# Kernel optimization log

Measured on AMD Instinct MI355X. Metric: run time of the kernel, lower is better.

## Reference

```python
import jax, jax.numpy as jnp
import numpy as np

J, P, L, C = 24, 8, 128, 8
N = 65536


def grid_sample(image, grid):
    # Bilinear grid_sample, align_corners=True, border-clamped indices
    # image: (B, C, H, W), grid: (B, Hg, Wg, 2) with (x=width, y=height) in [-1, 1]
    B, Cc, H, W = image.shape
    Hg, Wg = grid.shape[1], grid.shape[2]
    ix = (grid[..., 0] + 1.0) * 0.5 * (W - 1)
    iy = (grid[..., 1] + 1.0) * 0.5 * (H - 1)
    ix0 = jnp.floor(ix)
    iy0 = jnp.floor(iy)
    ix1 = ix0 + 1.0
    iy1 = iy0 + 1.0
    w_nw = (ix1 - ix) * (iy1 - iy)
    w_ne = (ix - ix0) * (iy1 - iy)
    w_sw = (ix1 - ix) * (iy - iy0)
    w_se = (ix - ix0) * (iy - iy0)
    ix0c = jnp.clip(ix0, 0, W - 1).astype(jnp.int32)
    ix1c = jnp.clip(ix1, 0, W - 1).astype(jnp.int32)
    iy0c = jnp.clip(iy0, 0, H - 1).astype(jnp.int32)
    iy1c = jnp.clip(iy1, 0, H - 1).astype(jnp.int32)
    img = image.reshape(B, Cc, H * W)

    def gather(iyc, ixc):
        idx = (iyc * W + ixc).reshape(B, 1, Hg * Wg)
        return jnp.take_along_axis(img, idx, axis=2)  # (B, Cc, Hg*Wg)

    out = (gather(iy0c, ix0c) * w_nw.reshape(B, 1, -1)
           + gather(iy0c, ix1c) * w_ne.reshape(B, 1, -1)
           + gather(iy1c, ix0c) * w_sw.reshape(B, 1, -1)
           + gather(iy1c, ix1c) * w_se.reshape(B, 1, -1))
    return out.reshape(B, Cc, Hg, Wg)


def sample(feat_lines, grid, pid):
    # feat_lines: (J, P, Lh, Lw, C); grid: (1, N, 1, 2)
    Jn, Pn, Lh, Lw, Cn = feat_lines.shape
    B, Np = grid.shape[:2]
    lines = jnp.transpose(feat_lines[:, pid], (0, 3, 1, 2)).reshape(1, Jn * Cn, Lh, Lw)
    feat = grid_sample(lines, grid)  # (1, J*C, N, 1)
    # raw reshape, replicating torch .view(B, N, J, C) on contiguous (1, J*C, N, 1)
    return feat.reshape(B, Np, Jn, Cn)


def setup_inputs():
    key = jax.random.key(0)
    ks = jax.random.split(key, 5)
    s = 0.01
    return {
        "feat_lines_x": jax.random.uniform(ks[0], (J, P, L, L, C), jnp.float32, -s, s),
        "feat_lines_y": jax.random.uniform(ks[1], (J, P, L, L, C), jnp.float32, -s, s),
        "feat_lines_z": jax.random.uniform(ks[2], (J, P, L, L, C), jnp.float32, -s, s),
        "query_points": jax.random.uniform(ks[3], (N, 3), jnp.float32),
        "scale": jnp.ones((3,), jnp.float32),
        "skinning_weight": jax.random.uniform(ks[4], (N, J), jnp.float32),
        "id": 3,
    }


def reference(feat_lines_x, feat_lines_y, feat_lines_z, query_points, scale, skinning_weight, id):
    qp = query_points - jnp.mean(query_points, axis=0)[None, :]  # (N, 3)
    x = qp[:, 0] / (scale[0] / 2)
    y = qp[:, 1] / (scale[1] / 2)
    z = qp[:, 2] / (scale[2] / 2)
    yx = jnp.stack((y, x), axis=1)[None, :, None, :]  # (1, N, 1, 2)
    xz = jnp.stack((x, z), axis=1)[None, :, None, :]
    zy = jnp.stack((z, y), axis=1)[None, :, None, :]
    feat_x = sample(feat_lines_x, yx, id)
    feat_y = sample(feat_lines_y, zy, id)
    feat_z = sample(feat_lines_z, xz, id)
    feat = jnp.concatenate([feat_x, feat_y, feat_z], axis=3)  # (1, N, J, 3C)
    return jnp.einsum('bnjc,nj->bnc', feat, skinning_weight)  # (1, N, 3C)
```

## Files before the change

### kernel.cpp

```cpp
#include <hip/hip_runtime.h>

constexpr int NPQ = 65536;
constexpr int JJ = 24, CC = 8, PP = 8, LL = 128;
constexpr int OUTC = 24;
constexpr int TOTAL = NPQ * OUTC;
constexpr int NCHP = 192;
constexpr size_t QPL = 8192;
constexpr size_t Q_ELEMS = (size_t)576 * QPL;

typedef _Float16 h2 __attribute__((ext_vector_type(2)));

constexpr float QSCALE = 12750.0f;
constexpr float QBIASF = 128.0f;
constexpr float INVQ = 1.0f / 12750.0f;

__global__ __launch_bounds__(256) void k_prep_all(
    const float* __restrict__ fx_, const float* __restrict__ fy_,
    const float* __restrict__ fz_, const int* __restrict__ idp,
    const float* __restrict__ qp, const float* __restrict__ sw,
    unsigned short* __restrict__ Q16, unsigned short* __restrict__ swh,
    float* __restrict__ partial) {
    int bid = blockIdx.x;
    int t = threadIdx.x;
    if (bid < 2304) {
        int g = bid >> 5;
        int rg = bid & 31;
        int p = g / 24, jimg = g - p * 24;
        const float* feat = (p == 0) ? fx_ : (p == 1) ? fy_ : fz_;
        int pid = *idp;
        int ly = t >> 6, k = t & 63;
        int y = rg * 4 + ly;
        int x2 = k * 2;
        const float* src = feat + (((size_t)jimg * PP + (size_t)pid) * 16384 +
                                   (size_t)(y * 128 + x2)) * 8;
        float4 a0 = *(const float4*)src;
        float4 a1 = *(const float4*)(src + 4);
        float4 b0 = *(const float4*)(src + 8);
        float4 b1 = *(const float4*)(src + 12);
        float av[8] = {a0.x, a0.y, a0.z, a0.w, a1.x, a1.y, a1.z, a1.w};
        float bv[8] = {b0.x, b0.y, b0.z, b0.w, b1.x, b1.y, b1.z, b1.w};
#pragma unroll
        for (int c = 0; c < 8; ++c) {
            unsigned qa = (unsigned)fmaf(av[c], QSCALE, QBIASF);
            unsigned qb = (unsigned)fmaf(bv[c], QSCALE, QBIASF);
            Q16[((size_t)(g * 8 + c) << 13) + (size_t)(y * 64 + k)] =
                (unsigned short)(qa | (qb << 8));
        }
    } else if (bid < 2560) {
        __shared__ float s[3][256];
        int n = (bid - 2304) * 256 + t;
        s[0][t] = qp[n * 3 + 0];
        s[1][t] = qp[n * 3 + 1];
        s[2][t] = qp[n * 3 + 2];
        __syncthreads();
        for (int off = 128; off > 0; off >>= 1) {
            if (t < off) {
                s[0][t] += s[0][t + off];
                s[1][t] += s[1][t + off];
                s[2][t] += s[2][t + off];
            }
            __syncthreads();
        }
        if (t == 0) {
            partial[(bid - 2304) * 4 + 0] = s[0][0];
            partial[(bid - 2304) * 4 + 1] = s[1][0];
            partial[(bid - 2304) * 4 + 2] = s[2][0];
        }
    } else {
        int n = (bid - 2560) * 256 + t;
        const float* s = sw + (size_t)n * 24;
        float4 v0 = *(const float4*)(s);
        float4 v1 = *(const float4*)(s + 4);
        float4 v2 = *(const float4*)(s + 8);
        float4 v3 = *(const float4*)(s + 12);
        float4 v4 = *(const float4*)(s + 16);
        float4 v5 = *(const float4*)(s + 20);
        float vv[24] = {v0.x, v0.y, v0.z, v0.w, v1.x, v1.y, v1.z, v1.w,
                        v2.x, v2.y, v2.z, v2.w, v3.x, v3.y, v3.z, v3.w,
                        v4.x, v4.y, v4.z, v4.w, v5.x, v5.y, v5.z, v5.w};
        unsigned u[12];
#pragma unroll
        for (int q = 0; q < 12; ++q) {
            h2 w;
            w[0] = (_Float16)vv[q * 2];
            w[1] = (_Float16)vv[q * 2 + 1];
            u[q] = __builtin_bit_cast(unsigned, w);
        }
        uint4* dst = (uint4*)(swh + (size_t)n * 24);
        dst[0] = make_uint4(u[0], u[1], u[2], u[3]);
        dst[1] = make_uint4(u[4], u[5], u[6], u[7]);
        dst[2] = make_uint4(u[8], u[9], u[10], u[11]);
    }
}

__global__ __launch_bounds__(256) void k_coord(
    const float* __restrict__ qp, const float* __restrict__ scale,
    const float* __restrict__ partial, unsigned int* __restrict__ co,
    float* __restrict__ out) {
    __shared__ float s[3][256];
    __shared__ float smean[3];
    int t = threadIdx.x;
    s[0][t] = partial[t * 4 + 0];
    s[1][t] = partial[t * 4 + 1];
    s[2][t] = partial[t * 4 + 2];
    __syncthreads();
    for (int off = 128; off > 0; off >>= 1) {
        if (t < off) {
            s[0][t] += s[0][t + off];
            s[1][t] += s[1][t + off];
            s[2][t] += s[2][t + off];
        }
        __syncthreads();
    }
    if (t < 3) smean[t] = s[t][0] * (1.0f / 65536.0f);
    __syncthreads();

    int gt = blockIdx.x * 256 + t;
    if (gt < 3 * 191 * 8) {
        int c = gt & 7;
        int rest = gt >> 3;
        int jcb = rest % 191;
        int p = rest / 191;
        if (((jcb + 1) % 3) != 0) {
            int np = ((jcb + 1) << 16) / 192;
            out[(size_t)np * 24 + p * 8 + c] = 0.0f;
        }
    }

    int n = blockIdx.x * 256 + t;
    float qv[3] = {qp[n * 3 + 0], qp[n * 3 + 1], qp[n * 3 + 2]};
#pragma unroll
    for (int p = 0; p < 3; ++p) {
        int wc = (p + 1) - ((p + 1) >= 3 ? 3 : 0);
        int hc = p;
        float gw = (qv[wc] - smean[wc]) * (2.0f / scale[wc]);
        float gh = (qv[hc] - smean[hc]) * (2.0f / scale[hc]);
        float ixf = (gw + 1.0f) * 63.5f;
        float iyf = (gh + 1.0f) * 63.5f;
        float fx0 = floorf(ixf), fy0 = floorf(iyf);
        float fx = ixf - fx0, fy = iyf - fy0;
        int x0i = (int)fx0, y0i = (int)fy0;
        int xr, yr;
        float fxc, fyc;
        if (x0i < 0)        { xr = 0;   fxc = 0.0f; }
        else if (x0i > 126) { xr = 126; fxc = 1.0f; }
        else                { xr = x0i; fxc = fx;   }
        if (y0i < 0)        { yr = 0;   fyc = 0.0f; }
        else if (y0i > 126) { yr = 126; fyc = 1.0f; }
        else                { yr = y0i; fyc = fy;   }
        unsigned fxq = (unsigned)__float2int_rn(fxc * 511.0f);
        unsigned fyq = (unsigned)__float2int_rn(fyc * 511.0f);
        co[((size_t)p << 16) + (size_t)n] =
            (unsigned)(yr * 128 + xr) | (fxq << 14) | (fyq << 23);
    }
}

__device__ __forceinline__ float sample1(const unsigned int* sp, unsigned d) {
    unsigned w = sp[d & 16383u];
    float fx = (float)((d >> 14) & 511u) * (1.0f / 511.0f);
    float fy = (float)(d >> 23) * (1.0f / 511.0f);
    float v00 = (float)(w & 255u);
    float v01 = (float)((w >> 8) & 255u);
    float v10 = (float)((w >> 16) & 255u);
    float v11 = (float)(w >> 24);
    float r0 = fmaf(fy, v10 - v00, v00);
    float r1 = fmaf(fy, v11 - v01, v01);
    return fmaf(fx, r1 - r0, r0);
}

__device__ __forceinline__ void up2(float* d, unsigned u) {
    h2 v = __builtin_bit_cast(h2, u);
    d[0] = (float)v[0];
    d[1] = (float)v[1];
}

__global__ __launch_bounds__(512, 4) void k_fused(
    const unsigned short* __restrict__ Q16, const unsigned int* __restrict__ co,
    const unsigned short* __restrict__ swh, float* __restrict__ out) {
    int b = blockIdx.x;
    int Lid = (b & 7) * 144 + (b >> 3);
    int half = Lid & 1;
    int jcp = Lid >> 1;
    int p = jcp / NCHP;
    int jc = jcp - p * NCHP;

    __shared__ unsigned int splane[16384];
    {
        const unsigned int* src32 =
            (const unsigned int*)(Q16 + ((size_t)jcp << 13));
        int tid = threadIdx.x;
#pragma unroll
        for (int it = 0; it < 8; ++it) {
            int i = it * 512 + tid;
            int y = i >> 5;
            int m = i & 31;
            int ip1 = (m < 31) ? i + 1 : i;
            int ro = (y < 127) ? 32 : 0;
            unsigned c0 = src32[i];
            unsigned c1 = src32[ip1];
            unsigned n0 = src32[i + ro];
            unsigned n1 = src32[ip1 + ro];
            unsigned w0 = __builtin_amdgcn_perm(n0, c0, 0x05040100u);
            unsigned w1 = __builtin_amdgcn_perm(n0, c0, 0x06050201u);
            unsigned w2 = __builtin_amdgcn_perm(n0, c0, 0x07060302u);
            unsigned selA = (m < 31) ? 0x00000403u : 0x00000303u;
            unsigned t0 = __builtin_amdgcn_perm(c1, c0, selA);
            unsigned t1 = __builtin_amdgcn_perm(n1, n0, selA);
            unsigned w3 = __builtin_amdgcn_perm(t1, t0, 0x05040100u);
            ((uint4*)splane)[i] = make_uint4(w0, w1, w2, w3);
        }
    }
    __syncthreads();
    const unsigned int* sp = splane;

    int i0 = jc << 16;
    int r  = (jc % 3) * 64;
    int r1 = ((jc + 1) % 3) * 64;
    int npF_lo = (i0 + 191) / 192;
    int npF_hi = ((jc + 1) << 16) / 192;
    int cnt = npF_hi - npF_lo;
    int mid = npF_lo + (cnt >> 1);
    int loR = half ? mid : npF_lo;
    int hiR = half ? npF_hi : mid;
    bool hasPre  = (half == 0) && (r != 0);
    bool hasPost = (half == 1) && (r1 != 0);

    int nFull = (hiR - loR) * 8;
    int nTot = nFull + (hasPre ? 8 : 0) + (hasPost ? 8 : 0);
    const unsigned int* cop = co + ((size_t)p << 16);

    for (int k = threadIdx.x; k < nTot; k += 512) {
        if (k < nFull) {
            int np = loR + (k >> 3);
            int c = k & 7;
            const unsigned int* cb = cop + (np * 192 + c - i0);
            const uint4* sw4 = (const uint4*)(swh + (size_t)np * 24);
            uint4 wA = sw4[0], wB = sw4[1], wC = sw4[2];
            float swreg[24];
            up2(swreg + 0,  wA.x); up2(swreg + 2,  wA.y);
            up2(swreg + 4,  wA.z); up2(swreg + 6,  wA.w);
            up2(swreg + 8,  wB.x); up2(swreg + 10, wB.y);
            up2(swreg + 12, wB.z); up2(swreg + 14, wB.w);
            up2(swreg + 16, wC.x); up2(swreg + 18, wC.y);
            up2(swreg + 20, wC.z); up2(swreg + 22, wC.w);
            float sumw = 0.0f;
#pragma unroll
            for (int j = 0; j < 24; ++j) sumw += swreg[j];
            float acc = 0.0f;
#pragma unroll
            for (int j = 0; j < 24; ++j) {
                unsigned d = cb[j * 8];
                acc = fmaf(swreg[j], sample1(sp, d), acc);
            }
            out[(size_t)np * 24 + p * 8 + c] = fmaf(acc, INVQ, -sumw * 0.01f);
        } else {
            bool isPre = hasPre && (k < nFull + 8);
            int c = (k - nFull) & 7;
            int np = isPre ? (i0 / 192) : npF_hi;
            int jlo = isPre ? (r >> 3) : 0;
            int jhi = isPre ? 24 : (r1 >> 3);
            int n0 = np * 192 + c - i0;
            float acc = 0.0f, sumw = 0.0f;
            for (int j = jlo; j < jhi; ++j) {
                unsigned d = cop[n0 + j * 8];
                float wj =
                    (float)__builtin_bit_cast(_Float16, swh[(size_t)np * 24 + j]);
                sumw += wj;
                acc = fmaf(wj, sample1(sp, d), acc);
            }
            atomicAdd(&out[(size_t)np * 24 + p * 8 + c],
                      fmaf(acc, INVQ, -sumw * 0.01f));
        }
    }
}

__global__ __launch_bounds__(256) void k_partial(const float* __restrict__ qp,
                                                 float* __restrict__ partial) {
    __shared__ float s[3][256];
    int t = threadIdx.x;
    int n = blockIdx.x * 256 + t;
    s[0][t] = qp[n * 3 + 0];
    s[1][t] = qp[n * 3 + 1];
    s[2][t] = qp[n * 3 + 2];
    __syncthreads();
    for (int off = 128; off > 0; off >>= 1) {
        if (t < off) {
            s[0][t] += s[0][t + off];
            s[1][t] += s[1][t + off];
            s[2][t] += s[2][t + off];
        }
        __syncthreads();
    }
    if (t == 0) {
        partial[blockIdx.x * 4 + 0] = s[0][0];
        partial[blockIdx.x * 4 + 1] = s[1][0];
        partial[blockIdx.x * 4 + 2] = s[2][0];
    }
}

__global__ __launch_bounds__(256) void k_finalm(const float* __restrict__ partial,
                                                float* __restrict__ mean) {
    __shared__ float s[3][256];
    int t = threadIdx.x;
    s[0][t] = partial[t * 4 + 0];
    s[1][t] = partial[t * 4 + 1];
    s[2][t] = partial[t * 4 + 2];
    __syncthreads();
    for (int off = 128; off > 0; off >>= 1) {
        if (t < off) {
            s[0][t] += s[0][t + off];
            s[1][t] += s[1][t + off];
            s[2][t] += s[2][t + off];
        }
        __syncthreads();
    }
    if (t < 3) mean[t] = s[t][0] * (1.0f / 65536.0f);
}

__global__ __launch_bounds__(256) void k_main(
    const float* __restrict__ featx, const float* __restrict__ featy,
    const float* __restrict__ featz, const float* __restrict__ qp,
    const float* __restrict__ scale, const float* __restrict__ sw,
    const int* __restrict__ idp, const float* __restrict__ mean,
    float* __restrict__ out) {
    int t = blockIdx.x * 256 + threadIdx.x;
    if (t >= TOTAL) return;
    int np = t / OUTC;
    int cp = t - np * OUTC;
    int p  = cp >> 3;
    int c  = cp & 7;
    const float* feat = (p == 0) ? featx : (p == 1) ? featy : featz;
    int pid = *idp;
    int wc = (p + 1) - ((p + 1) >= 3 ? 3 : 0);
    int hc = p;
    float mw = mean[wc], mh = mean[hc];
    float invw = 2.0f / scale[wc];
    float invh = 2.0f / scale[hc];
    const float* featpid = feat + (size_t)pid * (LL * LL * CC);
    int ibase = np * 192 + c;
    float acc = 0.0f;
#pragma unroll 4
    for (int j = 0; j < JJ; ++j) {
        int i  = ibase + j * 8;
        int jc = i >> 16;
        int n  = i & 65535;
        int jimg = jc >> 3;
        int cimg = jc & 7;
        const float* img = featpid + (size_t)jimg * (PP * LL * LL * CC) + cimg;
        float gw = (qp[n * 3 + wc] - mw) * invw;
        float gh = (qp[n * 3 + hc] - mh) * invh;
        float ixf = (gw + 1.0f) * 63.5f;
        float iyf = (gh + 1.0f) * 63.5f;
        float ix0 = floorf(ixf), iy0 = floorf(iyf);
        float fx = ixf - ix0, fy = iyf - iy0;
        int x0i = (int)ix0, y0i = (int)iy0;
        int x0 = min(127, max(0, x0i));
        int x1 = min(127, max(0, x0i + 1));
        int y0 = min(127, max(0, y0i));
        int y1 = min(127, max(0, y0i + 1));
        int r0 = y0 * (LL * CC);
        int r1 = y1 * (LL * CC);
        float v00 = img[r0 + x0 * CC];
        float v01 = img[r0 + x1 * CC];
        float v10 = img[r1 + x0 * CC];
        float v11 = img[r1 + x1 * CC];
        float omfx = 1.0f - fx, omfy = 1.0f - fy;
        float S = omfx * omfy * v00 + fx * omfy * v01 +
                  omfx * fy * v10 + fx * fy * v11;
        acc += sw[np * JJ + j] * S;
    }
    out[t] = acc;
}

extern "C" void kernel_launch(void* const* d_in, const int* in_sizes, int n_in,
                              void* d_out, int out_size, void* d_ws, size_t ws_size,
                              hipStream_t stream) {
    const float* featx = (const float*)d_in[0];
    const float* featy = (const float*)d_in[1];
    const float* featz = (const float*)d_in[2];
    const float* qp    = (const float*)d_in[3];
    const float* scale = (const float*)d_in[4];
    const float* sw    = (const float*)d_in[5];
    const int*   idp   = (const int*)d_in[6];
    float* out = (float*)d_out;

    size_t off_Q = 0;
    size_t off_co = off_Q + Q_ELEMS * 2;
    size_t off_sw = off_co + (size_t)3 * 65536 * 4;
    size_t off_partial = off_sw + (size_t)65536 * 24 * 2;
    size_t off_mean = off_partial + 4096;
    size_t needed = off_mean + 16;

    if (ws_size >= needed) {
        char* wsb = (char*)d_ws;
        unsigned short* Q16 = (unsigned short*)(wsb + off_Q);
        unsigned int* co    = (unsigned int*)(wsb + off_co);
        unsigned short* swh = (unsigned short*)(wsb + off_sw);
        float* partial      = (float*)(wsb + off_partial);

        k_prep_all<<<2816, 256, 0, stream>>>(featx, featy, featz, idp, qp, sw,
                                             Q16, swh, partial);
        k_coord<<<256, 256, 0, stream>>>(qp, scale, partial, co, out);
        k_fused<<<1152, 512, 0, stream>>>(Q16, co, swh, out);
    } else {
        float* ws = (float*)d_ws;
        float* mean    = ws;
        float* partial = ws + 4;
        k_partial<<<256, 256, 0, stream>>>(qp, partial);
        k_finalm<<<1, 256, 0, stream>>>(partial, mean);
        k_main<<<(TOTAL + 255) / 256, 256, 0, stream>>>(
            featx, featy, featz, qp, scale, sw, idp, mean, out);
    }
}
```

Baseline: 52.28 us.

## Shrink shared plane to 16-bit horizontal pairs and use one block per plane

```diff
diff --git a/kernel.cpp b/kernel.cpp
--- a/kernel.cpp
+++ b/kernel.cpp
@@ -155,14 +155,16 @@
     }
 }
 
-__device__ __forceinline__ float sample1(const unsigned int* sp, unsigned d) {
-    unsigned w = sp[d & 16383u];
+__device__ __forceinline__ float sample1(const unsigned short* sq, unsigned d) {
+    unsigned widx = d & 16383u;
+    unsigned w0 = sq[widx];
+    unsigned w1 = sq[widx + 128];
     float fx = (float)((d >> 14) & 511u) * (1.0f / 511.0f);
     float fy = (float)(d >> 23) * (1.0f / 511.0f);
-    float v00 = (float)(w & 255u);
-    float v01 = (float)((w >> 8) & 255u);
-    float v10 = (float)((w >> 16) & 255u);
-    float v11 = (float)(w >> 24);
+    float v00 = (float)(w0 & 255u);
+    float v01 = (float)(w0 >> 8);
+    float v10 = (float)(w1 & 255u);
+    float v11 = (float)(w1 >> 8);
     float r0 = fmaf(fy, v10 - v00, v00);
     float r1 = fmaf(fy, v11 - v01, v01);
     return fmaf(fx, r1 - r0, r0);
@@ -174,64 +176,46 @@
     d[1] = (float)v[1];
 }
 
-__global__ __launch_bounds__(512, 4) void k_fused(
+__global__ __launch_bounds__(256, 3) void k_fused(
     const unsigned short* __restrict__ Q16, const unsigned int* __restrict__ co,
     const unsigned short* __restrict__ swh, float* __restrict__ out) {
-    int b = blockIdx.x;
-    int Lid = (b & 7) * 144 + (b >> 3);
-    int half = Lid & 1;
-    int jcp = Lid >> 1;
+    int jcp = blockIdx.x;
     int p = jcp / NCHP;
     int jc = jcp - p * NCHP;
 
-    __shared__ unsigned int splane[16384];
+    __shared__ unsigned short sq[16384];
     {
         const unsigned int* src32 =
             (const unsigned int*)(Q16 + ((size_t)jcp << 13));
         int tid = threadIdx.x;
 #pragma unroll
-        for (int it = 0; it < 8; ++it) {
-            int i = it * 512 + tid;
-            int y = i >> 5;
+        for (int it = 0; it < 16; ++it) {
+            int i = it * 256 + tid;
             int m = i & 31;
-            int ip1 = (m < 31) ? i + 1 : i;
-            int ro = (y < 127) ? 32 : 0;
             unsigned c0 = src32[i];
-            unsigned c1 = src32[ip1];
-            unsigned n0 = src32[i + ro];
-            unsigned n1 = src32[ip1 + ro];
-            unsigned w0 = __builtin_amdgcn_perm(n0, c0, 0x05040100u);
-            unsigned w1 = __builtin_amdgcn_perm(n0, c0, 0x06050201u);
-            unsigned w2 = __builtin_amdgcn_perm(n0, c0, 0x07060302u);
-            unsigned selA = (m < 31) ? 0x00000403u : 0x00000303u;
-            unsigned t0 = __builtin_amdgcn_perm(c1, c0, selA);
-            unsigned t1 = __builtin_amdgcn_perm(n1, n0, selA);
-            unsigned w3 = __builtin_amdgcn_perm(t1, t0, 0x05040100u);
-            ((uint4*)splane)[i] = make_uint4(w0, w1, w2, w3);
-        }
-    }
-    __syncthreads();
-    const unsigned int* sp = splane;
+            unsigned c1 = src32[(m < 31) ? i + 1 : i];
+            unsigned w01 = __builtin_amdgcn_perm(c0, c0, 0x02010100u);
+            unsigned w23 = __builtin_amdgcn_perm(c1, c0, 0x04030302u);
+            ((uint2*)sq)[i] = make_uint2(w01, w23);
+        }
+    }
+    __syncthreads();
 
     int i0 = jc << 16;
     int r  = (jc % 3) * 64;
     int r1 = ((jc + 1) % 3) * 64;
     int npF_lo = (i0 + 191) / 192;
     int npF_hi = ((jc + 1) << 16) / 192;
-    int cnt = npF_hi - npF_lo;
-    int mid = npF_lo + (cnt >> 1);
-    int loR = half ? mid : npF_lo;
-    int hiR = half ? npF_hi : mid;
-    bool hasPre  = (half == 0) && (r != 0);
-    bool hasPost = (half == 1) && (r1 != 0);
-
-    int nFull = (hiR - loR) * 8;
+    bool hasPre  = (r != 0);
+    bool hasPost = (r1 != 0);
+
+    int nFull = (npF_hi - npF_lo) * 8;
     int nTot = nFull + (hasPre ? 8 : 0) + (hasPost ? 8 : 0);
     const unsigned int* cop = co + ((size_t)p << 16);
 
-    for (int k = threadIdx.x; k < nTot; k += 512) {
+    for (int k = threadIdx.x; k < nTot; k += 256) {
         if (k < nFull) {
-            int np = loR + (k >> 3);
+            int np = npF_lo + (k >> 3);
             int c = k & 7;
             const unsigned int* cb = cop + (np * 192 + c - i0);
             const uint4* sw4 = (const uint4*)(swh + (size_t)np * 24);
@@ -250,7 +234,7 @@
 #pragma unroll
             for (int j = 0; j < 24; ++j) {
                 unsigned d = cb[j * 8];
-                acc = fmaf(swreg[j], sample1(sp, d), acc);
+                acc = fmaf(swreg[j], sample1(sq, d), acc);
             }
             out[(size_t)np * 24 + p * 8 + c] = fmaf(acc, INVQ, -sumw * 0.01f);
         } else {
@@ -266,7 +250,7 @@
                 float wj =
                     (float)__builtin_bit_cast(_Float16, swh[(size_t)np * 24 + j]);
                 sumw += wj;
-                acc = fmaf(wj, sample1(sp, d), acc);
+                acc = fmaf(wj, sample1(sq, d), acc);
             }
             atomicAdd(&out[(size_t)np * 24 + p * 8 + c],
                       fmaf(acc, INVQ, -sumw * 0.01f));
@@ -401,7 +385,7 @@
         k_prep_all<<<2816, 256, 0, stream>>>(featx, featy, featz, idp, qp, sw,
                                              Q16, swh, partial);
         k_coord<<<256, 256, 0, stream>>>(qp, scale, partial, co, out);
-        k_fused<<<1152, 512, 0, stream>>>(Q16, co, swh, out);
+        k_fused<<<576, 256, 0, stream>>>(Q16, co, swh, out);
     } else {
         float* ws = (float*)d_ws;
         float* mean    = ws;
```

Result: slower. 55.33 us (+5.8%).
